# Kernel optimization log

Measured on AMD Instinct MI355X. Metric: run time of the kernel, lower is better.

## Reference

```python
import jax, jax.numpy as jnp
import numpy as np


def setup_inputs() -> dict:
    key = jax.random.key(0)
    k1, k2 = jax.random.split(key)
    hw, bs, c = 16384, 16, 256
    nq = 100
    return {
        "query_feat": jax.random.normal(k1, (hw, bs, c), dtype=jnp.float32),
        "support_feat": jax.random.normal(k2, (nq, bs, c), dtype=jnp.float32),
        "h": 128,
        "w": 128,
    }


def reference(query_feat, support_feat, h, w):
    # query_feat: [hw, bs, c], support_feat: [nq, bs, c]
    hw, bs, c = query_feat.shape
    nq = support_feat.shape[0]
    dtype = query_feat.dtype

    side_normalizer = jnp.array([w, h], dtype=dtype)[None, None, :]  # [1,1,2]

    q = jnp.transpose(query_feat, (1, 0, 2))    # [bs, hw, c]
    s = jnp.transpose(support_feat, (1, 0, 2))  # [bs, nq, c]

    # bmm(q, s^T) -> [bs, hw, nq]; transpose -> [bs, nq, hw]
    similarity_flat = jnp.einsum('bnc,bkc->bnk', s, q)        # [bs, nq, hw]
    similarity = similarity_flat.reshape(bs, nq, h, w)

    # coordinate grid: stack([grid_x, grid_y]) with 'ij' meshgrid, flattened to [hw, 2]
    ys = jnp.linspace(0.5, h - 0.5, h, dtype=jnp.float32)
    xs = jnp.linspace(0.5, w - 0.5, w, dtype=jnp.float32)
    grid_y, grid_x = jnp.meshgrid(ys, xs, indexing='ij')      # [h, w] each
    coord = jnp.stack([grid_x, grid_y], axis=-1).reshape(hw, 2)  # [hw, 2]

    similarity_softmax = jax.nn.softmax(similarity_flat, axis=-1)  # [bs, nq, hw]

    proposal_for_loss = jnp.einsum('bnk,kd->bnd', similarity_softmax, coord) / side_normalizer

    # peak masking: argmax -> one_hot -> reshape (w, h) [faithful to original swap] -> 3x3 max pool
    max_pos = jnp.argmax(similarity_flat, axis=-1)            # [bs, nq]
    max_mask = jax.nn.one_hot(max_pos, hw, dtype=jnp.float32).reshape(bs, nq, w, h)
    local_max_mask = jax.lax.reduce_window(
        max_mask, -jnp.inf, jax.lax.max,
        window_dimensions=(1, 1, 3, 3), window_strides=(1, 1, 1, 1),
        padding=((0, 0), (0, 0), (1, 1), (1, 1)),
    ).reshape(bs, nq, hw)                                     # [bs, nq, hw]

    local_sm = similarity_softmax * local_max_mask            # [bs, nq, hw]
    local_sm = local_sm / (jnp.sum(local_sm, axis=-1, keepdims=True) + 1e-10)
    proposals = jnp.einsum('bnk,kd->bnd', local_sm, coord) / side_normalizer

    return (proposal_for_loss, similarity, proposals)
```

## Files before the change

### kernel.cpp

```cpp
#include <hip/hip_runtime.h>
#include <math.h>

#define HW   16384
#define BS   16
#define C    256
#define NQ   100
#define NQP  112
#define Hh   128
#define Ww   128

#define SIM_OFF   3200
#define PROPS_OFF (3200 + 26214400)

#define BM 256
#define BK 32
#define NBLK (HW / BM)

typedef _Float16 half8 __attribute__((ext_vector_type(8)));
typedef float f32x4 __attribute__((ext_vector_type(4)));

__device__ __forceinline__ void gll16(const void* gp, void* lp) {
    __builtin_amdgcn_global_load_lds((const __attribute__((address_space(1))) void*)gp,
                                     (__attribute__((address_space(3))) void*)lp, 16, 0, 0);
}

__device__ __forceinline__ half8 cvt8(const float4 a, const float4 b) {
    _Float16 h[8] = {(_Float16)a.x, (_Float16)a.y, (_Float16)a.z, (_Float16)a.w,
                     (_Float16)b.x, (_Float16)b.y, (_Float16)b.z, (_Float16)b.w};
    return *(half8*)h;
}

__global__ __launch_bounds__(256) void conv_S_kernel(const float* __restrict__ S,
                                                     _Float16* __restrict__ sh)
{
    int idx4 = blockIdx.x * 256 + threadIdx.x;
    int idx = idx4 * 4;
    if (idx >= BS * NQP * C) return;
    int b = idx / (NQP * C);
    int rem = idx - b * (NQP * C);
    int n = rem / C;
    int k = rem - n * C;
    float4 v = make_float4(0.f, 0.f, 0.f, 0.f);
    if (n < NQ) v = *(const float4*)(S + ((size_t)n * BS + b) * C + k);
    _Float16 h[4] = {(_Float16)v.x, (_Float16)v.y, (_Float16)v.z, (_Float16)v.w};
    *(uint2*)(sh + idx) = *(uint2*)h;
}

template<bool USE_WS>
__global__ __launch_bounds__(256, 2) void gemm_kernel(const float* __restrict__ Q,
                                                      const float* __restrict__ S,
                                                      const _Float16* __restrict__ ShG,
                                                      float* __restrict__ out,
                                                      float* __restrict__ pm,
                                                      float* __restrict__ pz,
                                                      float* __restrict__ pwx,
                                                      float* __restrict__ pwy,
                                                      int* __restrict__ pidx)
{
    __shared__ __align__(16) float    Qf[BM * BK];
    __shared__ __align__(16) _Float16 SH[NQP * BK];
    __shared__ __align__(16) float Ws[NQP][4][4];

    const int b    = blockIdx.y;
    const int hw0  = blockIdx.x * BM;
    const int t    = threadIdx.x;
    const int wid  = t >> 6;
    const int lane = t & 63;
    const int lr   = lane & 15;
    const int lg   = lane >> 4;

    f32x4 acc[4][7];
    #pragma unroll
    for (int am = 0; am < 4; ++am)
        #pragma unroll
        for (int bn = 0; bn < 7; ++bn)
            acc[am][bn] = (f32x4)(0.f);

    const int q_r8 = lane >> 3;
    const int q_gc = (lane & 7) ^ q_r8;
    const int s_r  = lane >> 2;
    const int s_gc = (lane & 3) ^ ((lane >> 3) & 3);

    for (int k0 = 0; k0 < C; k0 += BK) {
        #pragma unroll
        for (int p = 0; p < 8; ++p) {
            int rt = wid * 64 + p * 8;
            const float* g = Q + ((size_t)(hw0 + rt + q_r8) * BS + b) * C + k0 + q_gc * 4;
            gll16(g, &Qf[rt * BK]);
        }
        if (USE_WS) {
            for (int i = wid; i < 7; i += 4) {
                int r0 = i * 16;
                const _Float16* g = ShG + ((size_t)b * NQP + r0 + s_r) * C + k0 + s_gc * 8;
                gll16(g, &SH[r0 * BK]);
            }
        }
        __syncthreads();

        half8 qh[4];
        #pragma unroll
        for (int am = 0; am < 4; ++am) {
            int row = wid * 64 + 16 * am + lr;
            int r7 = row & 7;
            float4 qa = *(const float4*)&Qf[row * BK + (((2 * lg + 0) ^ r7) << 2)];
            float4 qb = *(const float4*)&Qf[row * BK + (((2 * lg + 1) ^ r7) << 2)];
            qh[am] = cvt8(qa, qb);
        }

        #pragma unroll
        for (int bn = 0; bn < 7; ++bn) {
            int row = 16 * bn + lr;
            half8 sh;
            if (USE_WS) {
                int slot = lg ^ ((row >> 1) & 3);
                sh = *(const half8*)&SH[row * BK + slot * 8];
            } else {
                if (row < NQ) {
                    const float* g = S + ((size_t)row * BS + b) * C + k0 + 8 * lg;
                    float4 sa = *(const float4*)g;
                    float4 sb = *(const float4*)(g + 4);
                    sh = cvt8(sa, sb);
                } else {
                    sh = (half8)(_Float16)0.f;
                }
            }
            #pragma unroll
            for (int am = 0; am < 4; ++am)
                acc[am][bn] = __builtin_amdgcn_mfma_f32_16x16x32_f16(qh[am], sh, acc[am][bn], 0, 0, 0);
        }
        __syncthreads();
    }

    float* simb = out + SIM_OFF;
    const int hwl0 = wid * 64 + 4 * lg;
    #pragma unroll
    for (int bn = 0; bn < 7; ++bn) {
        int nq = 16 * bn + lr;
        if (nq < NQ) {
            size_t rbase = ((size_t)(b * NQ + nq)) * HW + hw0 + hwl0;
            #pragma unroll
            for (int am = 0; am < 4; ++am)
                *(float4*)&simb[rbase + 16 * am] =
                    make_float4(acc[am][bn][0], acc[am][bn][1], acc[am][bn][2], acc[am][bn][3]);
        }
        if (USE_WS) {
            float vm = acc[0][bn][0];
            int   ci = hwl0;
            #pragma unroll
            for (int am = 0; am < 4; ++am)
                #pragma unroll
                for (int j = 0; j < 4; ++j) {
                    float v = acc[am][bn][j];
                    if (v > vm) { vm = v; ci = hwl0 + 16 * am + j; }
                }
            float z = 0.f, wx = 0.f;
            #pragma unroll
            for (int am = 0; am < 4; ++am)
                #pragma unroll
                for (int j = 0; j < 4; ++j) {
                    float e = __expf(acc[am][bn][j] - vm);
                    z += e;
                    wx += e * ((float)((hwl0 + 16 * am + j) & 127) + 0.5f);
                }
            #pragma unroll
            for (int off = 16; off < 64; off <<= 1) {
                float om = __shfl_xor(vm, off);
                int   oc = __shfl_xor(ci, off);
                float oz = __shfl_xor(z, off);
                float ox = __shfl_xor(wx, off);
                bool take = (om > vm) || (om == vm && oc < ci);
                float mn = take ? om : vm;
                float ss = __expf(vm - mn);
                float so = __expf(om - mn);
                z  = z * ss + oz * so;
                wx = wx * ss + ox * so;
                vm = mn;
                ci = take ? oc : ci;
            }
            if (lg == 0) {
                f32x4 tu = {vm, __int_as_float(ci), z, wx};
                *(f32x4*)&Ws[nq][wid][0] = tu;
            }
        }
    }
    if (USE_WS) {
        __syncthreads();
        if (t < NQ) {
            int nq = t;
            float M = -3.4e38f; int gi = 0;
            float mw[4], zw[4], xw[4]; int cw[4];
            #pragma unroll
            for (int w = 0; w < 4; ++w) {
                f32x4 tu = *(const f32x4*)&Ws[nq][w][0];
                mw[w] = tu[0]; cw[w] = __float_as_int(tu[1]); zw[w] = tu[2]; xw[w] = tu[3];
                if (mw[w] > M || (mw[w] == M && cw[w] < gi)) { M = mw[w]; gi = cw[w]; }
            }
            float ybase = (float)(hw0 >> 7) + 0.5f;
            float Zp = 0.f, WXp = 0.f, WYp = 0.f;
            #pragma unroll
            for (int w = 0; w < 4; ++w) {
                float s = __expf(mw[w] - M);
                Zp  += zw[w] * s;
                WXp += xw[w] * s;
                WYp += zw[w] * s * (ybase + (float)(w >> 1));
            }
            size_t pbase = ((size_t)b * NBLK + blockIdx.x) * NQ + nq;
            pm[pbase] = M; pz[pbase] = Zp; pwx[pbase] = WXp; pwy[pbase] = WYp;
            pidx[pbase] = hw0 + gi;
        }
    }
}

__global__ __launch_bounds__(256) void finalize_kernel(const float* __restrict__ sim,
                                                       const float* __restrict__ pm,
                                                       const float* __restrict__ pz,
                                                       const float* __restrict__ pwx,
                                                       const float* __restrict__ pwy,
                                                       const int* __restrict__ pidx,
                                                       float* __restrict__ out)
{
    const int rglob = blockIdx.x * 4 + (threadIdx.x >> 6);
    const int lane  = threadIdx.x & 63;
    const int b     = rglob / NQ;
    const int n     = rglob - b * NQ;
    const size_t base = ((size_t)b * NBLK + lane) * NQ + n;

    float m  = pm[base];
    float z  = pz[base];
    float wx = pwx[base];
    float wy = pwy[base];
    int   gi = pidx[base];

    float v = m; int vi = gi;
    #pragma unroll
    for (int off = 1; off < 64; off <<= 1) {
        float ov = __shfl_xor(v, off);
        int   oi = __shfl_xor(vi, off);
        if (ov > v || (ov == v && oi < vi)) { v = ov; vi = oi; }
    }
    float s  = __expf(m - v);
    float Z  = z * s;
    float WX = wx * s;
    float WY = wy * s;
    #pragma unroll
    for (int off = 1; off < 64; off <<= 1) {
        Z  += __shfl_xor(Z, off);
        WX += __shfl_xor(WX, off);
        WY += __shfl_xor(WY, off);
    }
    if (lane == 0) {
        out[(size_t)rglob * 2 + 0] = (WX / Z) * (1.f / 128.f);
        out[(size_t)rglob * 2 + 1] = (WY / Z) * (1.f / 128.f);
        const float* srow = sim + (size_t)rglob * HW;
        int pr = vi >> 7, pc = vi & 127;
        float ls = 0.f, lx = 0.f, ly = 0.f;
        #pragma unroll
        for (int dr = -1; dr <= 1; ++dr) {
            #pragma unroll
            for (int dc = -1; dc <= 1; ++dc) {
                int r = pr + dr, c = pc + dc;
                if (r >= 0 && r < Ww && c >= 0 && c < Hh) {
                    int k = r * Hh + c;
                    float e = __expf(srow[k] - v);
                    ls += e;
                    lx += e * ((float)(k & 127) + 0.5f);
                    ly += e * ((float)(k >> 7) + 0.5f);
                }
            }
        }
        float denom = ls + 1e-10f * Z;
        out[PROPS_OFF + (size_t)rglob * 2 + 0] = (lx / denom) * (1.f / 128.f);
        out[PROPS_OFF + (size_t)rglob * 2 + 1] = (ly / denom) * (1.f / 128.f);
    }
}

__global__ __launch_bounds__(256) void reduce_kernel(const float* __restrict__ sim,
                                                     float* __restrict__ out)
{
    __shared__ float rowbuf[HW];
    __shared__ float s_pm[4];
    __shared__ int   s_pi[4];
    __shared__ float s_red[4][3];
    __shared__ float s_gmax;
    __shared__ int   s_gidx;

    const int row = blockIdx.x;
    const int t   = threadIdx.x;
    const int wid  = t >> 6;
    const int lane = t & 63;
    const float4* src4 = (const float4*)(sim + (size_t)row * HW);

    float vmax = -3.4e38f;
    int   vidx = 0;
    #pragma unroll
    for (int p = 0; p < 16; ++p) {
        int i4 = p * 256 + t;
        float4 v = src4[i4];
        *(float4*)&rowbuf[i4 * 4] = v;
        int base = i4 * 4;
        if (v.x > vmax) { vmax = v.x; vidx = base; }
        if (v.y > vmax) { vmax = v.y; vidx = base + 1; }
        if (v.z > vmax) { vmax = v.z; vidx = base + 2; }
        if (v.w > vmax) { vmax = v.w; vidx = base + 3; }
    }
    #pragma unroll
    for (int off = 32; off > 0; off >>= 1) {
        float ov = __shfl_down(vmax, off);
        int   oi = __shfl_down(vidx, off);
        if (ov > vmax || (ov == vmax && oi < vidx)) { vmax = ov; vidx = oi; }
    }
    if (lane == 0) { s_pm[wid] = vmax; s_pi[wid] = vidx; }
    __syncthreads();
    if (t == 0) {
        float gm = s_pm[0]; int gi = s_pi[0];
        #pragma unroll
        for (int wv = 1; wv < 4; ++wv) {
            float ov = s_pm[wv]; int oi = s_pi[wv];
            if (ov > gm || (ov == gm && oi < gi)) { gm = ov; gi = oi; }
        }
        s_gmax = gm; s_gidx = gi;
    }
    __syncthreads();
    const float gmax = s_gmax;

    float z = 0.f, wx = 0.f, wy = 0.f;
    #pragma unroll
    for (int p = 0; p < 16; ++p) {
        int i4 = p * 256 + t;
        float4 v = *(const float4*)&rowbuf[i4 * 4];
        int i = i4 * 4;
        float e0 = __expf(v.x - gmax), e1 = __expf(v.y - gmax);
        float e2 = __expf(v.z - gmax), e3 = __expf(v.w - gmax);
        z += (e0 + e1) + (e2 + e3);
        float cy = (float)(i >> 7) + 0.5f;
        float cx0 = (float)(i & (Ww - 1)) + 0.5f;
        wx += e0 * cx0 + e1 * (cx0 + 1.f) + e2 * (cx0 + 2.f) + e3 * (cx0 + 3.f);
        wy += (e0 + e1 + e2 + e3) * cy;
    }
    #pragma unroll
    for (int off = 32; off > 0; off >>= 1) {
        z  += __shfl_down(z, off);
        wx += __shfl_down(wx, off);
        wy += __shfl_down(wy, off);
    }
    if (lane == 0) { s_red[wid][0] = z; s_red[wid][1] = wx; s_red[wid][2] = wy; }
    __syncthreads();

    if (t == 0) {
        float Z = 0.f, WX = 0.f, WY = 0.f;
        #pragma unroll
        for (int wv = 0; wv < 4; ++wv) { Z += s_red[wv][0]; WX += s_red[wv][1]; WY += s_red[wv][2]; }

        out[(size_t)row * 2 + 0] = (WX / Z) * (1.0f / (float)Ww);
        out[(size_t)row * 2 + 1] = (WY / Z) * (1.0f / (float)Hh);

        int p  = s_gidx;
        int pr = p / Hh;
        int pc = p % Hh;
        float lsum = 0.f, lwx = 0.f, lwy = 0.f;
        #pragma unroll
        for (int di = -1; di <= 1; ++di) {
            #pragma unroll
            for (int dj = -1; dj <= 1; ++dj) {
                int r = pr + di, c = pc + dj;
                if (r >= 0 && r < Ww && c >= 0 && c < Hh) {
                    int k = r * Hh + c;
                    float e = __expf(rowbuf[k] - gmax);
                    lsum += e;
                    lwx  += e * ((float)(k & (Ww - 1)) + 0.5f);
                    lwy  += e * ((float)(k >> 7) + 0.5f);
                }
            }
        }
        float denom = lsum + 1e-10f * Z;
        out[PROPS_OFF + (size_t)row * 2 + 0] = (lwx / denom) * (1.0f / (float)Ww);
        out[PROPS_OFF + (size_t)row * 2 + 1] = (lwy / denom) * (1.0f / (float)Hh);
    }
}

extern "C" void kernel_launch(void* const* d_in, const int* in_sizes, int n_in,
                              void* d_out, int out_size, void* d_ws, size_t ws_size,
                              hipStream_t stream) {
    const float* Q = (const float*)d_in[0];
    const float* S = (const float*)d_in[1];
    float* out = (float*)d_out;

    const size_t splitElems = (size_t)BS * NQP * C;
    const size_t splitBytes = splitElems * sizeof(_Float16);
    const size_t nPart = (size_t)BS * NQ * NBLK;
    const size_t pOff  = (splitBytes + 255) & ~(size_t)255;
    const size_t wsNeeded = pOff + nPart * 5 * sizeof(float);

    if (ws_size >= wsNeeded) {
        _Float16* sh = (_Float16*)d_ws;
        float* pm  = (float*)((char*)d_ws + pOff);
        float* pz  = pm + nPart;
        float* pwx = pz + nPart;
        float* pwy = pwx + nPart;
        int*   pidx = (int*)(pwy + nPart);
        conv_S_kernel<<<dim3((unsigned)((splitElems / 4 + 255) / 256)), 256, 0, stream>>>(S, sh);
        gemm_kernel<true><<<dim3(HW / BM, BS), 256, 0, stream>>>(Q, S, sh, out,
                                                                 pm, pz, pwx, pwy, pidx);
        finalize_kernel<<<dim3(BS * NQ / 4), 256, 0, stream>>>(out + SIM_OFF, pm, pz, pwx, pwy, pidx, out);
    } else {
        gemm_kernel<false><<<dim3(HW / BM, BS), 256, 0, stream>>>(Q, S, nullptr, out,
                                                                  nullptr, nullptr, nullptr, nullptr, nullptr);
        reduce_kernel<<<dim3(BS * NQ), 256, 0, stream>>>(out + SIM_OFF, out);
    }
}
```

Before: 108.9 us.

## Double-buffer LDS tiles in GEMM so global loads overlap MFMA compute

Splits the Q and S shared-memory tiles into two buffers. The next K-slice is prefetched with global_load_lds while MFMAs run on the current slice, and one wait plus one barrier per iteration replaces the previous pair of __syncthreads. The aim is to hide the global-load latency of the streaming Q reads behind compute. The LDS footprint roughly doubles, so the per-block reduction scratch now aliases the Q buffer after the loop. The larger footprint may limit how many blocks fit per CU under the 2-block launch bound.

```diff
diff --git a/kernel.cpp b/kernel.cpp
--- a/kernel.cpp
+++ b/kernel.cpp
@@ -57,9 +57,8 @@
                                                       float* __restrict__ pwy,
                                                       int* __restrict__ pidx)
 {
-    __shared__ __align__(16) float    Qf[BM * BK];
-    __shared__ __align__(16) _Float16 SH[NQP * BK];
-    __shared__ __align__(16) float Ws[NQP][4][4];
+    __shared__ __align__(16) float    Qf[2][BM * BK];
+    __shared__ __align__(16) _Float16 SH[2][NQP * BK];
 
     const int b    = blockIdx.y;
     const int hw0  = blockIdx.x * BM;
@@ -81,29 +80,46 @@
     const int s_r  = lane >> 2;
     const int s_gc = (lane & 3) ^ ((lane >> 3) & 3);
 
-    for (int k0 = 0; k0 < C; k0 += BK) {
+    auto stageQ = [&](int buf, int k0) {
         #pragma unroll
         for (int p = 0; p < 8; ++p) {
             int rt = wid * 64 + p * 8;
             const float* g = Q + ((size_t)(hw0 + rt + q_r8) * BS + b) * C + k0 + q_gc * 4;
-            gll16(g, &Qf[rt * BK]);
-        }
-        if (USE_WS) {
-            for (int i = wid; i < 7; i += 4) {
-                int r0 = i * 16;
-                const _Float16* g = ShG + ((size_t)b * NQP + r0 + s_r) * C + k0 + s_gc * 8;
-                gll16(g, &SH[r0 * BK]);
-            }
-        }
-        __syncthreads();
+            gll16(g, &Qf[buf][rt * BK]);
+        }
+    };
+    auto stageS = [&](int buf, int k0) {
+        for (int i = wid; i < 7; i += 4) {
+            int r0 = i * 16;
+            const _Float16* g = ShG + ((size_t)b * NQP + r0 + s_r) * C + k0 + s_gc * 8;
+            gll16(g, &SH[buf][r0 * BK]);
+        }
+    };
+
+    stageQ(0, 0);
+    if (USE_WS) stageS(0, 0);
+    asm volatile("s_waitcnt vmcnt(0)" ::: "memory");
+    __builtin_amdgcn_sched_barrier(0);
+    __builtin_amdgcn_s_barrier();
+    __builtin_amdgcn_sched_barrier(0);
+
+    #pragma unroll
+    for (int k = 0; k < 8; ++k) {
+        const int cur = k & 1;
+        const int k0  = k * BK;
+
+        if (k < 7) {
+            stageQ(cur ^ 1, k0 + BK);
+            if (USE_WS) stageS(cur ^ 1, k0 + BK);
+        }
 
         half8 qh[4];
         #pragma unroll
         for (int am = 0; am < 4; ++am) {
             int row = wid * 64 + 16 * am + lr;
             int r7 = row & 7;
-            float4 qa = *(const float4*)&Qf[row * BK + (((2 * lg + 0) ^ r7) << 2)];
-            float4 qb = *(const float4*)&Qf[row * BK + (((2 * lg + 1) ^ r7) << 2)];
+            float4 qa = *(const float4*)&Qf[cur][row * BK + (((2 * lg + 0) ^ r7) << 2)];
+            float4 qb = *(const float4*)&Qf[cur][row * BK + (((2 * lg + 1) ^ r7) << 2)];
             qh[am] = cvt8(qa, qb);
         }
 
@@ -113,7 +129,7 @@
             half8 sh;
             if (USE_WS) {
                 int slot = lg ^ ((row >> 1) & 3);
-                sh = *(const half8*)&SH[row * BK + slot * 8];
+                sh = *(const half8*)&SH[cur][row * BK + slot * 8];
             } else {
                 if (row < NQ) {
                     const float* g = S + ((size_t)row * BS + b) * C + k0 + 8 * lg;
@@ -128,8 +144,17 @@
             for (int am = 0; am < 4; ++am)
                 acc[am][bn] = __builtin_amdgcn_mfma_f32_16x16x32_f16(qh[am], sh, acc[am][bn], 0, 0, 0);
         }
-        __syncthreads();
-    }
+
+        if (k < 7) {
+            asm volatile("s_waitcnt vmcnt(0)" ::: "memory");
+            __builtin_amdgcn_sched_barrier(0);
+            __builtin_amdgcn_s_barrier();
+            __builtin_amdgcn_sched_barrier(0);
+        }
+    }
+
+    __syncthreads();
+    float* Ws = (float*)&Qf[0][0];
 
     float* simb = out + SIM_OFF;
     const int hwl0 = wid * 64 + 4 * lg;
@@ -179,7 +204,7 @@
             }
             if (lg == 0) {
                 f32x4 tu = {vm, __int_as_float(ci), z, wx};
-                *(f32x4*)&Ws[nq][wid][0] = tu;
+                *(f32x4*)&Ws[(nq * 4 + wid) * 4] = tu;
             }
         }
     }
@@ -191,7 +216,7 @@
             float mw[4], zw[4], xw[4]; int cw[4];
             #pragma unroll
             for (int w = 0; w < 4; ++w) {
-                f32x4 tu = *(const f32x4*)&Ws[nq][w][0];
+                f32x4 tu = *(const f32x4*)&Ws[(nq * 4 + w) * 4];
                 mw[w] = tu[0]; cw[w] = __float_as_int(tu[1]); zw[w] = tu[2]; xw[w] = tu[3];
                 if (mw[w] > M || (mw[w] == M && cw[w] < gi)) { M = mw[w]; gi = cw[w]; }
             }
```

Result: no change. 109.2 us (+0.3%).

## Double K tile to 64, remap block ids so batches share Q rows, reuse LDS for Ws

Applied to the files above, without the earlier changes.

Doubles the K chunk per iteration from 32 to 64, which halves the number of barrier-separated load/compute rounds. The swizzle patterns for Q and S shared-memory tiles are redone to match the wider rows. The grid becomes 1D, with a remapping that groups all batches for the same 8 hw tiles together. Because Q is laid out [hw, bs, c], blocks for different batches at the same hw rows touch adjacent memory and may share cache lines. The Ws reduction buffer now aliases the SH tile to offset the larger shared-memory footprint (about 72KB), though that may still limit occupancy to 2 blocks per CU.

```diff
diff --git a/kernel.cpp b/kernel.cpp
--- a/kernel.cpp
+++ b/kernel.cpp
@@ -13,7 +13,7 @@
 #define PROPS_OFF (3200 + 26214400)
 
 #define BM 256
-#define BK 32
+#define BK 64
 #define NBLK (HW / BM)
 
 typedef _Float16 half8 __attribute__((ext_vector_type(8)));
@@ -59,10 +59,14 @@
 {
     __shared__ __align__(16) float    Qf[BM * BK];
     __shared__ __align__(16) _Float16 SH[NQP * BK];
-    __shared__ __align__(16) float Ws[NQP][4][4];
-
-    const int b    = blockIdx.y;
-    const int hw0  = blockIdx.x * BM;
+
+    const int id  = blockIdx.x;
+    const int xc  = id & 7;
+    const int m_  = id >> 3;
+    const int b   = m_ & 15;
+    const int x   = ((m_ >> 4) << 3) | xc;
+    const int hw0 = x * BM;
+
     const int t    = threadIdx.x;
     const int wid  = t >> 6;
     const int lane = t & 63;
@@ -76,60 +80,65 @@
         for (int bn = 0; bn < 7; ++bn)
             acc[am][bn] = (f32x4)(0.f);
 
-    const int q_r8 = lane >> 3;
-    const int q_gc = (lane & 7) ^ q_r8;
-    const int s_r  = lane >> 2;
-    const int s_gc = (lane & 3) ^ ((lane >> 3) & 3);
+    const int q_ri = lane >> 4;
+    const int s_ri = lane >> 3;
+    const int s_gc = (lane & 7) ^ s_ri;
 
     for (int k0 = 0; k0 < C; k0 += BK) {
         #pragma unroll
-        for (int p = 0; p < 8; ++p) {
-            int rt = wid * 64 + p * 8;
-            const float* g = Q + ((size_t)(hw0 + rt + q_r8) * BS + b) * C + k0 + q_gc * 4;
+        for (int p = 0; p < 16; ++p) {
+            int rt  = wid * 64 + p * 4;
+            int r15 = (p * 4 + q_ri) & 15;
+            int gc  = (lane & 15) ^ r15;
+            const float* g = Q + ((size_t)(hw0 + rt + q_ri) * BS + b) * C + k0 + gc * 4;
             gll16(g, &Qf[rt * BK]);
         }
         if (USE_WS) {
-            for (int i = wid; i < 7; i += 4) {
-                int r0 = i * 16;
-                const _Float16* g = ShG + ((size_t)b * NQP + r0 + s_r) * C + k0 + s_gc * 8;
+            for (int i = wid; i < 14; i += 4) {
+                int r0 = i * 8;
+                const _Float16* g = ShG + ((size_t)b * NQP + r0 + s_ri) * C + k0 + s_gc * 8;
                 gll16(g, &SH[r0 * BK]);
             }
         }
         __syncthreads();
 
-        half8 qh[4];
-        #pragma unroll
-        for (int am = 0; am < 4; ++am) {
-            int row = wid * 64 + 16 * am + lr;
-            int r7 = row & 7;
-            float4 qa = *(const float4*)&Qf[row * BK + (((2 * lg + 0) ^ r7) << 2)];
-            float4 qb = *(const float4*)&Qf[row * BK + (((2 * lg + 1) ^ r7) << 2)];
-            qh[am] = cvt8(qa, qb);
-        }
-
-        #pragma unroll
-        for (int bn = 0; bn < 7; ++bn) {
-            int row = 16 * bn + lr;
-            half8 sh;
-            if (USE_WS) {
-                int slot = lg ^ ((row >> 1) & 3);
-                sh = *(const half8*)&SH[row * BK + slot * 8];
-            } else {
-                if (row < NQ) {
-                    const float* g = S + ((size_t)row * BS + b) * C + k0 + 8 * lg;
-                    float4 sa = *(const float4*)g;
-                    float4 sb = *(const float4*)(g + 4);
-                    sh = cvt8(sa, sb);
+        #pragma unroll
+        for (int s = 0; s < 2; ++s) {
+            half8 qh[4];
+            #pragma unroll
+            for (int am = 0; am < 4; ++am) {
+                int row = wid * 64 + 16 * am + lr;
+                int c0  = 8 * s + 2 * lg;
+                float4 qa = *(const float4*)&Qf[row * BK + (((c0)     ^ lr) << 2)];
+                float4 qb = *(const float4*)&Qf[row * BK + (((c0 + 1) ^ lr) << 2)];
+                qh[am] = cvt8(qa, qb);
+            }
+            #pragma unroll
+            for (int bn = 0; bn < 7; ++bn) {
+                int row = 16 * bn + lr;
+                half8 sh;
+                if (USE_WS) {
+                    int sl = (4 * s + lg) ^ (row & 7);
+                    sh = *(const half8*)&SH[row * BK + sl * 8];
                 } else {
-                    sh = (half8)(_Float16)0.f;
+                    if (row < NQ) {
+                        const float* g = S + ((size_t)row * BS + b) * C + k0 + 32 * s + 8 * lg;
+                        float4 sa = *(const float4*)g;
+                        float4 sb = *(const float4*)(g + 4);
+                        sh = cvt8(sa, sb);
+                    } else {
+                        sh = (half8)(_Float16)0.f;
+                    }
                 }
-            }
-            #pragma unroll
-            for (int am = 0; am < 4; ++am)
-                acc[am][bn] = __builtin_amdgcn_mfma_f32_16x16x32_f16(qh[am], sh, acc[am][bn], 0, 0, 0);
+                #pragma unroll
+                for (int am = 0; am < 4; ++am)
+                    acc[am][bn] = __builtin_amdgcn_mfma_f32_16x16x32_f16(qh[am], sh, acc[am][bn], 0, 0, 0);
+            }
         }
         __syncthreads();
     }
+
+    float* Ws = (float*)&SH[0];
 
     float* simb = out + SIM_OFF;
     const int hwl0 = wid * 64 + 4 * lg;
@@ -179,7 +188,7 @@
             }
             if (lg == 0) {
                 f32x4 tu = {vm, __int_as_float(ci), z, wx};
-                *(f32x4*)&Ws[nq][wid][0] = tu;
+                *(f32x4*)&Ws[(nq * 4 + wid) * 4] = tu;
             }
         }
     }
@@ -191,7 +200,7 @@
             float mw[4], zw[4], xw[4]; int cw[4];
             #pragma unroll
             for (int w = 0; w < 4; ++w) {
-                f32x4 tu = *(const f32x4*)&Ws[nq][w][0];
+                f32x4 tu = *(const f32x4*)&Ws[(nq * 4 + w) * 4];
                 mw[w] = tu[0]; cw[w] = __float_as_int(tu[1]); zw[w] = tu[2]; xw[w] = tu[3];
                 if (mw[w] > M || (mw[w] == M && cw[w] < gi)) { M = mw[w]; gi = cw[w]; }
             }
@@ -204,7 +213,7 @@
                 WXp += xw[w] * s;
                 WYp += zw[w] * s * (ybase + (float)(w >> 1));
             }
-            size_t pbase = ((size_t)b * NBLK + blockIdx.x) * NQ + nq;
+            size_t pbase = ((size_t)b * NBLK + x) * NQ + nq;
             pm[pbase] = M; pz[pbase] = Zp; pwx[pbase] = WXp; pwy[pbase] = WYp;
             pidx[pbase] = hw0 + gi;
         }
@@ -399,12 +408,12 @@
         float* pwy = pwx + nPart;
         int*   pidx = (int*)(pwy + nPart);
         conv_S_kernel<<<dim3((unsigned)((splitElems / 4 + 255) / 256)), 256, 0, stream>>>(S, sh);
-        gemm_kernel<true><<<dim3(HW / BM, BS), 256, 0, stream>>>(Q, S, sh, out,
-                                                                 pm, pz, pwx, pwy, pidx);
+        gemm_kernel<true><<<dim3(HW / BM * BS), 256, 0, stream>>>(Q, S, sh, out,
+                                                                  pm, pz, pwx, pwy, pidx);
         finalize_kernel<<<dim3(BS * NQ / 4), 256, 0, stream>>>(out + SIM_OFF, pm, pz, pwx, pwy, pidx, out);
     } else {
-        gemm_kernel<false><<<dim3(HW / BM, BS), 256, 0, stream>>>(Q, S, nullptr, out,
-                                                                  nullptr, nullptr, nullptr, nullptr, nullptr);
+        gemm_kernel<false><<<dim3(HW / BM * BS), 256, 0, stream>>>(Q, S, nullptr, out,
+                                                                   nullptr, nullptr, nullptr, nullptr, nullptr);
         reduce_kernel<<<dim3(BS * NQ), 256, 0, stream>>>(out + SIM_OFF, out);
     }
 }
```

New measurement: 101.6 us. 6.7% less time.
